# Kernel tuning notes

Measured on AMD Instinct MI355X. Metric: run time of the kernel, lower is better.

Reference implementation:

```python
import jax, jax.numpy as jnp
import numpy as np

N, E, G = 50000, 800000, 64
F_IN, H, R, C = 64, 64, 3, 10


def setup_inputs() -> dict:
    key = jax.random.key(0)
    ks = jax.random.split(key, 16)
    s = 0.1
    return dict(
        x=jax.random.normal(ks[0], (N, F_IN), jnp.float32),
        edge_index=jax.random.randint(ks[1], (2, E), 0, N, dtype=jnp.int32),
        edge_type=jax.random.randint(ks[2], (E,), 0, R, dtype=jnp.int32),
        graph_batch=jnp.sort(jax.random.randint(ks[3], (N,), 0, G, dtype=jnp.int32)),
        # FiLMConv params (per-relation lin: bias=False; per-relation film: bias=True)
        film_lin_W=jax.random.normal(ks[4], (R, F_IN, H), jnp.float32) * s,
        film_film_W=jax.random.normal(ks[5], (R, F_IN, 2 * H), jnp.float32) * s,
        film_film_b=jnp.zeros((R, 2 * H), jnp.float32),
        skip_W=jax.random.normal(ks[6], (F_IN, H), jnp.float32) * s,
        skip_film_W=jax.random.normal(ks[7], (F_IN, 2 * H), jnp.float32) * s,
        skip_film_b=jnp.zeros((2 * H,), jnp.float32),
        # GATConv params (heads=1, concat=True, lin bias=False, final bias=True)
        gat_W=jax.random.normal(ks[8], (F_IN, H), jnp.float32) * s,
        gat_att_src=jax.random.normal(ks[9], (H,), jnp.float32) * s,
        gat_att_dst=jax.random.normal(ks[10], (H,), jnp.float32) * s,
        gat_b=jnp.zeros((H,), jnp.float32),
        # classifier MLP
        lin_W=jax.random.normal(ks[11], (4 * H, H), jnp.float32) * s,
        lin_b=jnp.zeros((H,), jnp.float32),
        fc_W=jax.random.normal(ks[12], (H, C), jnp.float32) * s,
        fc_b=jnp.zeros((C,), jnp.float32),
    )


def _film_conv(x, edge_index, edge_type, lin_W, film_W, film_b,
               skip_W, skip_film_W, skip_film_b):
    # PyG FiLMConv, aggr='mean' per relation, act=relu.
    n, r, h = x.shape[0], lin_W.shape[0], skip_W.shape[1]
    src, dst = edge_index[0], edge_index[1]
    fs = x @ skip_film_W + skip_film_b                  # [N,2H]; split -> (beta, gamma)
    out = jax.nn.relu(fs[:, h:] * (x @ skip_W) + fs[:, :h])
    xr = jnp.einsum('nd,rdh->rnh', x, lin_W)            # [R,N,H]
    fm = jnp.einsum('nd,rdh->rnh', x, film_W) + film_b[:, None, :]  # [R,N,2H]
    beta, gamma = fm[..., :h], fm[..., h:]
    # each edge uses its own relation's lin/film params
    msg = jax.nn.relu(gamma[edge_type, dst] * xr[edge_type, src] + beta[edge_type, dst])  # [E,H]
    seg = dst * r + edge_type                            # per-(node,relation) mean
    cnt = jax.ops.segment_sum(jnp.ones_like(msg[:, 0]), seg, num_segments=n * r)
    denom = jnp.maximum(cnt[seg], 1.0)
    agg = jax.ops.segment_sum(msg / denom[:, None], dst, num_segments=n)
    return out + agg


def _gat_conv(x, edge_index, W, att_src, att_dst, b):
    # PyG GATConv, heads=1, negative_slope=0.2, add_self_loops=True.
    n = x.shape[0]
    xp = x @ W                                           # [N,H]
    loop = jnp.arange(n, dtype=edge_index.dtype)
    src = jnp.concatenate([edge_index[0], loop])
    dst = jnp.concatenate([edge_index[1], loop])
    e = jax.nn.leaky_relu((xp @ att_src)[src] + (xp @ att_dst)[dst], 0.2)  # [E+N]
    m = jax.ops.segment_max(e, dst, num_segments=n)
    alpha = jnp.exp(e - m[dst])
    denom = jax.ops.segment_sum(alpha, dst, num_segments=n)
    alpha = alpha / denom[dst]
    return jax.ops.segment_sum(alpha[:, None] * xp[src], dst, num_segments=n) + b


def reference(x, edge_index, edge_type, graph_batch,
              film_lin_W, film_film_W, film_film_b, skip_W, skip_film_W, skip_film_b,
              gat_W, gat_att_src, gat_att_dst, gat_b,
              lin_W, lin_b, fc_W, fc_b):
    out1 = jax.nn.relu(_film_conv(x, edge_index, edge_type, film_lin_W, film_film_W,
                                  film_film_b, skip_W, skip_film_W, skip_film_b))
    out2 = jax.nn.relu(_gat_conv(x, edge_index, gat_W, gat_att_src, gat_att_dst, gat_b))
    feats = jnp.concatenate([out1, out2], axis=-1)       # [N,2H]
    g = G
    cnt = jax.ops.segment_sum(jnp.ones_like(feats[:, 0]), graph_batch, num_segments=g)
    mx = jax.ops.segment_max(feats, graph_batch, num_segments=g)
    mx = jnp.where(cnt[:, None] > 0, mx, 0.0)
    mean = jax.ops.segment_sum(feats, graph_batch, num_segments=g) / jnp.maximum(cnt, 1.0)[:, None]
    pooled = jnp.concatenate([mx, mean], axis=-1)        # [G,4H]
    hidden = jax.nn.relu(pooled @ lin_W + lin_b)         # dropout = identity (eval)
    logits = hidden @ fc_W + fc_b
    return jax.nn.log_softmax(logits, axis=-1)
```

## Files before the change

### kernel.cpp

```cpp
#include <hip/hip_runtime.h>
#include <hip/hip_bf16.h>

#define NN 50000
#define EE 800000
#define GG 64
#define RR 3
#define CC 10
#define RPL 16
#define NBG 782
#define NBS 1563

typedef __attribute__((ext_vector_type(8))) short bf16x8;
typedef __attribute__((ext_vector_type(4))) float f32x4;

__device__ inline float leaky02(float x) { return x > 0.f ? x : 0.2f * x; }

__device__ inline void atomicMaxFPos(float* addr, float v) {
  atomicMax((int*)addr, __float_as_int(v));
}

__device__ inline unsigned short f2bf(float f) {
  __hip_bfloat16 b = __float2bfloat16(f);
  return *reinterpret_cast<unsigned short*>(&b);
}
__device__ inline float bf2f(unsigned short u) {
  return __uint_as_float(((unsigned int)u) << 16);
}

__global__ void wpack_k(const float* __restrict__ skip_film_W,
                        const float* __restrict__ skip_W,
                        const float* __restrict__ film_lin_W,
                        const float* __restrict__ film_film_W,
                        const float* __restrict__ gat_W,
                        const float* __restrict__ skip_film_b,
                        const float* __restrict__ film_film_b,
                        unsigned short* __restrict__ Wt,
                        float* __restrict__ bias) {
  int idx = blockIdx.x * 256 + threadIdx.x;
  if (idx >= 832 * 64 + 832) return;
  if (idx >= 832 * 64) {
    int c = idx - 832 * 64;
    float bv = 0.f;
    if (c < 128) bv = skip_film_b[c];
    else if (c >= 384 && c < 768) bv = film_film_b[c - 384];
    bias[c] = bv;
    return;
  }
  int c = idx >> 6, k = idx & 63;
  float v;
  if (c < 128)      v = skip_film_W[k * 128 + c];
  else if (c < 192) v = skip_W[k * 64 + (c - 128)];
  else if (c < 384) { int cc = c - 192, r = cc >> 6, h = cc & 63;
                      v = film_lin_W[(r * 64 + k) * 64 + h]; }
  else if (c < 768) { int cc = c - 384, r = cc >> 7, j = cc & 127;
                      v = film_film_W[(r * 64 + k) * 128 + j]; }
  else              v = gat_W[k * 64 + (c - 768)];
  Wt[idx] = f2bf(v);
}

__global__ __launch_bounds__(256) void fuse_k(const float* __restrict__ X,
    const unsigned short* __restrict__ Wt, const float* __restrict__ bias,
    const float* __restrict__ att_src, const float* __restrict__ att_dst,
    unsigned short* __restrict__ XP, unsigned short* __restrict__ XR,
    unsigned short* __restrict__ Ybg,
    unsigned short* __restrict__ S0b, float* __restrict__ as_,
    float* __restrict__ ad_,
    const int* __restrict__ ei, const int* __restrict__ et,
    int* __restrict__ fill4, int* __restrict__ sorted) {
  __shared__ __align__(16) unsigned short As[64][72];
  __shared__ __align__(16) unsigned short Bs[128][72];
  const int tid = threadIdx.x;

  if (blockIdx.x >= NBG) {
    int e = (blockIdx.x - NBG) * 512 + tid * 2;
    if (e < EE) {
      int2 s2 = *reinterpret_cast<const int2*>(ei + e);
      int2 d2 = *reinterpret_cast<const int2*>(ei + EE + e);
      int2 t2 = *reinterpret_cast<const int2*>(et + e);
      int slot = atomicAdd(&fill4[d2.x * 4 + t2.x], 1);
      if (slot < 32) sorted[d2.x * 96 + t2.x * 32 + slot] = s2.x;
      slot = atomicAdd(&fill4[d2.y * 4 + t2.y], 1);
      if (slot < 32) sorted[d2.y * 96 + t2.y * 32 + slot] = s2.y;
    }
    return;
  }

  const int row0 = blockIdx.x * 64;
  {
    int r = tid >> 2, c0 = (tid & 3) * 16;
    int gr = row0 + r;
    ushort4 o0 = {0,0,0,0}, o1 = {0,0,0,0}, o2 = {0,0,0,0}, o3 = {0,0,0,0};
    if (gr < NN) {
      const float4* p = reinterpret_cast<const float4*>(X + (size_t)gr * 64 + c0);
      float4 v0 = p[0], v1 = p[1], v2 = p[2], v3 = p[3];
      o0 = {f2bf(v0.x), f2bf(v0.y), f2bf(v0.z), f2bf(v0.w)};
      o1 = {f2bf(v1.x), f2bf(v1.y), f2bf(v1.z), f2bf(v1.w)};
      o2 = {f2bf(v2.x), f2bf(v2.y), f2bf(v2.z), f2bf(v2.w)};
      o3 = {f2bf(v3.x), f2bf(v3.y), f2bf(v3.z), f2bf(v3.w)};
    }
    *reinterpret_cast<ushort4*>(&As[r][c0])      = o0;
    *reinterpret_cast<ushort4*>(&As[r][c0 + 4])  = o1;
    *reinterpret_cast<ushort4*>(&As[r][c0 + 8])  = o2;
    *reinterpret_cast<ushort4*>(&As[r][c0 + 12]) = o3;
  }
  __syncthreads();

  const int w = tid >> 6, lane = tid & 63;
  const int m = lane & 15, q = lane >> 4;
  bf16x8 a0 = *reinterpret_cast<const bf16x8*>(&As[16 * w + m][q * 8]);
  bf16x8 a1 = *reinterpret_cast<const bf16x8*>(&As[16 * w + m][32 + q * 8]);
  const int rbase = row0 + 16 * w + q * 4;

  f32x4 t0[8], t1[4], t6[4];

  for (int tile = 0; tile < 7; tile++) {
    __syncthreads();
    int col0 = tile * 128;
    int width = (tile == 6) ? 64 : 128;
    {
      int c = tid >> 1, half = (tid & 1) * 32;
      if (c < width) {
        int gc = col0 + c;
        const uint4* p = reinterpret_cast<const uint4*>(Wt + (size_t)gc * 64 + half);
        uint4 v0 = p[0], v1 = p[1], v2 = p[2], v3 = p[3];
        *reinterpret_cast<uint4*>(&Bs[c][half])      = v0;
        *reinterpret_cast<uint4*>(&Bs[c][half + 8])  = v1;
        *reinterpret_cast<uint4*>(&Bs[c][half + 16]) = v2;
        *reinterpret_cast<uint4*>(&Bs[c][half + 24]) = v3;
      }
    }
    __syncthreads();
    #pragma unroll
    for (int ct = 0; ct < 8; ct++) {
      if (tile == 6 && ct >= 4) continue;
      bf16x8 b0 = *reinterpret_cast<const bf16x8*>(&Bs[ct * 16 + m][q * 8]);
      bf16x8 b1 = *reinterpret_cast<const bf16x8*>(&Bs[ct * 16 + m][32 + q * 8]);
      f32x4 acc = {0.f, 0.f, 0.f, 0.f};
      acc = __builtin_amdgcn_mfma_f32_16x16x32_bf16(a0, b0, acc, 0, 0, 0);
      acc = __builtin_amdgcn_mfma_f32_16x16x32_bf16(a1, b1, acc, 0, 0, 0);
      if (tile == 0) { t0[ct] = acc; continue; }
      if (tile == 1 && ct < 4) { t1[ct] = acc; continue; }
      if (tile == 6) t6[ct] = acc;
      int colm = ct * 16 + m;
      float bv = (tile >= 3 && tile <= 5) ? bias[col0 + colm] : 0.f;
      #pragma unroll
      for (int rg = 0; rg < 4; rg++) {
        int gr = rbase + rg;
        if (gr >= NN) continue;
        float v = acc[rg];
        if (tile == 1) {
          XR[(size_t)gr * 64 + (colm - 64)] = f2bf(v);
        } else if (tile == 2) {
          if (ct < 4) XR[((size_t)NN + gr) * 64 + colm]            = f2bf(v);
          else        XR[((size_t)2 * NN + gr) * 64 + (colm - 64)] = f2bf(v);
        } else if (tile <= 5) {
          Ybg[(size_t)gr * 384 + (col0 - 384) + colm] = f2bf(v + bv);
        } else {
          XP[(size_t)gr * 64 + colm] = f2bf(v);
        }
      }
    }
  }

  float pa[4] = {0.f, 0.f, 0.f, 0.f}, pd[4] = {0.f, 0.f, 0.f, 0.f};
  #pragma unroll
  for (int j = 0; j < 4; j++) {
    int h = 16 * j + m;
    float bb = bias[h];
    float bg = bias[64 + h];
    float asv = att_src[h];
    float adv = att_dst[h];
    #pragma unroll
    for (int rg = 0; rg < 4; rg++) {
      float so = fmaxf((t0[4 + j][rg] + bg) * t1[j][rg] + (t0[j][rg] + bb), 0.f);
      int gr = rbase + rg;
      if (gr < NN) S0b[(size_t)gr * 64 + h] = f2bf(so);
      pa[rg] += t6[j][rg] * asv;
      pd[rg] += t6[j][rg] * adv;
    }
  }
  #pragma unroll
  for (int ofs = 1; ofs < 16; ofs <<= 1) {
    #pragma unroll
    for (int rg = 0; rg < 4; rg++) {
      pa[rg] += __shfl_xor(pa[rg], ofs);
      pd[rg] += __shfl_xor(pd[rg], ofs);
    }
  }
  if (m == 0) {
    #pragma unroll
    for (int rg = 0; rg < 4; rg++) {
      int gr = rbase + rg;
      if (gr < NN) { as_[gr] = pa[rg]; ad_[gr] = pd[rg]; }
    }
  }
}

#define RPN 16

__global__ __launch_bounds__(256) void dst_k(const int* __restrict__ sorted,
    const int* __restrict__ fill4, const unsigned short* __restrict__ XP,
    const unsigned short* __restrict__ XR,
    const unsigned short* __restrict__ Ybg,
    const unsigned short* __restrict__ S0b,
    const float* __restrict__ as_, const float* __restrict__ ad_,
    const float* __restrict__ gat_b, const int* __restrict__ gb,
    float* __restrict__ pmax, float* __restrict__ psum,
    int* __restrict__ gstart, int* __restrict__ gend) {
  __shared__ int   s_pk[4][96];
  __shared__ float s_w [4][96];
  __shared__ int   s_d [4][4];
  __shared__ int   s_g[4];
  __shared__ float s_ad[4];
  __shared__ __align__(16) unsigned short s_rows[64][128];
  float* s_val = (float*)&s_rows[0][0];

  const int tid = threadIdx.x;
  const int wid = tid >> 6, h = tid & 63;
  const int n0 = blockIdx.x * 4;
  const int n  = n0 + wid;

  size_t rep = (size_t)(blockIdx.x & (RPL - 1)) * GG * 128;
  pmax += rep; psum += rep;

  if (tid < 16) {
    int wd = tid >> 2, t = tid & 3;
    if (t < 3) {
      int d = fill4[(n0 + wd) * 4 + t];
      s_d[wd][t] = d > 32 ? 32 : d;
    } else {
      s_g[wd]  = gb[n0 + wd];
      s_ad[wd] = ad_[n0 + wd];
    }
  }
  __syncthreads();

  for (int i = tid; i < 512; i += 256) {
    int wd = i >> 7, s = i & 127;
    if (s < 96) {
      int tt = s >> 5, j = s & 31;
      if (j < s_d[wd][tt]) {
        int cidx = (tt == 0) ? j
                 : (tt == 1) ? s_d[wd][0] + j
                             : s_d[wd][0] + s_d[wd][1] + j;
        int src = sorted[(size_t)(n0 + wd) * 96 + s];
        s_pk[wd][cidx] = src;
        s_w[wd][cidx]  = leaky02(as_[src] + s_ad[wd]);
      }
    }
  }
  __syncthreads();

  const int d0 = s_d[wid][0], d1 = s_d[wid][1], d2 = s_d[wid][2];
  const int sB = d0 + d1;
  const int deg = sB + d2;
  const float adn = s_ad[wid];
  float es = leaky02(as_[n] + adn);

  bool v1 = h < deg;
  bool v2 = h + 64 < deg;
  float e1 = v1 ? s_w[wid][h]      : -1e30f;
  float e2 = v2 ? s_w[wid][64 + h] : -1e30f;
  float mg = fmaxf(fmaxf(e1, e2), es);
  #pragma unroll
  for (int ofs = 1; ofs < 64; ofs <<= 1) mg = fmaxf(mg, __shfl_xor(mg, ofs));
  float w1 = v1 ? __expf(e1 - mg) : 0.f;
  float w2 = v2 ? __expf(e2 - mg) : 0.f;
  if (v1) s_w[wid][h] = w1;
  if (v2) s_w[wid][64 + h] = w2;
  float den = w1 + w2;
  #pragma unroll
  for (int ofs = 1; ofs < 64; ofs <<= 1) den += __shfl_xor(den, ofs);
  float ws = __expf(es - mg);
  den += ws;

  const float i0 = 1.f / (float)(d0 > 1 ? d0 : 1);
  const float i1 = 1.f / (float)(d1 > 1 ? d1 : 1);
  const float i2 = 1.f / (float)(d2 > 1 ? d2 : 1);
  const unsigned short* ybg = Ybg + (size_t)n * 384;
  const float b0p = bf2f(ybg[h])       * i0, g0p = bf2f(ybg[64 + h])  * i0;
  const float b1p = bf2f(ybg[128 + h]) * i1, g1p = bf2f(ybg[192 + h]) * i1;
  const float b2p = bf2f(ybg[256 + h]) * i2, g2p = bf2f(ybg[320 + h]) * i2;

  float S = ws * bf2f(XP[(size_t)n * 64 + h]);
  float f = 0.f;

  const int grp16 = tid >> 4, lane16 = tid & 15;
  int kA[4], kB[4], kD[4];
  #pragma unroll
  for (int k = 0; k < 4; k++) {
    kA[k] = s_d[k][0];
    kB[k] = kA[k] + s_d[k][1];
    kD[k] = kB[k] + s_d[k][2];
  }
  int dmax = max(max(kD[0], kD[1]), max(kD[2], kD[3]));
  int rounds = (dmax + RPN - 1) / RPN;

  for (int r = 0; r < rounds; r++) {
    int e0 = r * RPN;
    #pragma unroll
    for (int k = 0; k < 4; k++) {
      int jj = e0 + grp16;
      if (jj < kD[k]) {
        int src = s_pk[k][jj];
        int t = jj < kA[k] ? 0 : (jj < kB[k] ? 1 : 2);
        const unsigned short* row = (lane16 < 8)
            ? XP + (size_t)src * 64 + lane16 * 8
            : XR + ((size_t)t * NN + src) * 64 + (lane16 - 8) * 8;
        uint4 v = *reinterpret_cast<const uint4*>(row);
        *reinterpret_cast<uint4*>(&s_rows[16 * k + grp16][lane16 * 8]) = v;
      }
    }
    __syncthreads();
    const unsigned short* rowp = &s_rows[wid * RPN][0];
    int hi0 = min(e0 + RPN, d0);
    for (int i = e0; i < hi0; i++) {
      float wj = s_w[wid][i];
      int sr = i - e0;
      float xp = bf2f(rowp[sr * 128 + h]);
      float xr = bf2f(rowp[sr * 128 + 64 + h]);
      S += wj * xp;
      f += fmaxf(g0p * xr + b0p, 0.f);
    }
    int lo1 = max(e0, d0), hi1 = min(e0 + RPN, sB);
    for (int i = lo1; i < hi1; i++) {
      float wj = s_w[wid][i];
      int sr = i - e0;
      float xp = bf2f(rowp[sr * 128 + h]);
      float xr = bf2f(rowp[sr * 128 + 64 + h]);
      S += wj * xp;
      f += fmaxf(g1p * xr + b1p, 0.f);
    }
    int lo2 = max(e0, sB), hi2 = min(e0 + RPN, deg);
    for (int i = lo2; i < hi2; i++) {
      float wj = s_w[wid][i];
      int sr = i - e0;
      float xp = bf2f(rowp[sr * 128 + h]);
      float xr = bf2f(rowp[sr * 128 + 64 + h]);
      S += wj * xp;
      f += fmaxf(g2p * xr + b2p, 0.f);
    }
    __syncthreads();
  }

  float o1 = fmaxf(bf2f(S0b[(size_t)n * 64 + h]) + f, 0.f);
  float o2 = fmaxf(S / den + gat_b[h], 0.f);

  s_val[wid * 128 + h]      = o1;
  s_val[wid * 128 + 64 + h] = o2;
  if (h == 0) {
    int g = s_g[wid];
    if (n == 0 || gb[n - 1] != g)      gstart[g] = n;
    if (n == NN - 1 || gb[n + 1] != g) gend[g] = n;
  }
  __syncthreads();
  if (tid < 128) {
    int fch = tid;
    int curg = s_g[0];
    float v0 = s_val[fch];
    float mx = v0, sm = v0;
    #pragma unroll
    for (int j = 1; j < 4; j++) {
      float v = s_val[j * 128 + fch];
      if (s_g[j] == curg) { mx = fmaxf(mx, v); sm += v; }
      else {
        atomicMaxFPos(&pmax[curg * 128 + fch], mx);
        atomicAdd(&psum[curg * 128 + fch], sm);
        curg = s_g[j]; mx = v; sm = v;
      }
    }
    atomicMaxFPos(&pmax[curg * 128 + fch], mx);
    atomicAdd(&psum[curg * 128 + fch], sm);
  }
}

__global__ __launch_bounds__(64) void head_k(const float* __restrict__ pmax,
    const float* __restrict__ psum, const int* __restrict__ gstart,
    const int* __restrict__ gend,
    const float* __restrict__ lin_W, const float* __restrict__ lin_b,
    const float* __restrict__ fc_W, const float* __restrict__ fc_b,
    float* __restrict__ out) {
  __shared__ float p[256];
  __shared__ float hid[64];
  __shared__ float lg[CC];
  __shared__ float lse;
  int g = blockIdx.x, t = threadIdx.x;
  int s = gstart[g], e = gend[g];
  int cnt = (s <= e && s < NN && s >= 0) ? (e - s + 1) : 0;
  float invc = 1.f / (float)(cnt > 1 ? cnt : 1);
  for (int i = t; i < 256; i += 64) {
    if (i < 128) {
      float mx = 0.f;
      for (int r = 0; r < RPL; r++)
        mx = fmaxf(mx, pmax[((size_t)r * GG + g) * 128 + i]);
      p[i] = mx;
    } else {
      int f = i - 128;
      float sm = 0.f;
      for (int r = 0; r < RPL; r++)
        sm += psum[((size_t)r * GG + g) * 128 + f];
      p[i] = sm * invc;
    }
  }
  __syncthreads();
  float acc = lin_b[t];
  for (int k = 0; k < 256; k++) acc += p[k] * lin_W[k * 64 + t];
  hid[t] = fmaxf(acc, 0.f);
  __syncthreads();
  if (t < CC) {
    float a = fc_b[t];
    for (int k = 0; k < 64; k++) a += hid[k] * fc_W[k * CC + t];
    lg[t] = a;
  }
  __syncthreads();
  if (t == 0) {
    float mx = lg[0];
    for (int i = 1; i < CC; i++) mx = fmaxf(mx, lg[i]);
    float sum = 0.f;
    for (int i = 0; i < CC; i++) sum += expf(lg[i] - mx);
    lse = mx + logf(sum);
  }
  __syncthreads();
  if (t < CC) out[g * CC + t] = lg[t] - lse;
}

extern "C" void kernel_launch(void* const* d_in, const int* in_sizes, int n_in,
                              void* d_out, int out_size, void* d_ws, size_t ws_size,
                              hipStream_t stream) {
  const float* x            = (const float*)d_in[0];
  const int*   edge_index   = (const int*)d_in[1];
  const int*   edge_type    = (const int*)d_in[2];
  const int*   graph_batch  = (const int*)d_in[3];
  const float* film_lin_W   = (const float*)d_in[4];
  const float* film_film_W  = (const float*)d_in[5];
  const float* film_film_b  = (const float*)d_in[6];
  const float* skip_W       = (const float*)d_in[7];
  const float* skip_film_W  = (const float*)d_in[8];
  const float* skip_film_b  = (const float*)d_in[9];
  const float* gat_W        = (const float*)d_in[10];
  const float* att_src      = (const float*)d_in[11];
  const float* att_dst      = (const float*)d_in[12];
  const float* gat_b        = (const float*)d_in[13];
  const float* lin_W        = (const float*)d_in[14];
  const float* lin_b        = (const float*)d_in[15];
  const float* fc_W         = (const float*)d_in[16];
  const float* fc_b         = (const float*)d_in[17];
  float* out                = (float*)d_out;

  float* ws = (float*)d_ws;
  const size_t N = NN, G = GG;
  size_t oXP     = 0;
  size_t oXR     = N * 32;
  size_t oYbg    = oXR + N * 96;
  size_t oS0     = oYbg + N * 192;
  size_t oAs     = oS0 + N * 32;
  size_t oAd     = oAs + N;
  size_t oWt     = oAd + N;
  size_t oBias   = oWt + 832 * 32;
  size_t oPmax   = oBias + 832;
  size_t oPsum   = oPmax + (size_t)RPL * G * 128;
  size_t oGend   = oPsum + (size_t)RPL * G * 128;
  size_t oFill   = oGend + G;
  size_t oGstart = oFill + N * 4;
  size_t oSorted = oGstart + G;

  unsigned short* XP  = (unsigned short*)(ws + oXP);
  unsigned short* XR  = (unsigned short*)(ws + oXR);
  unsigned short* Ybg = (unsigned short*)(ws + oYbg);
  unsigned short* S0b = (unsigned short*)(ws + oS0);
  float* as_    = ws + oAs;
  float* ad_    = ws + oAd;
  unsigned short* Wt  = (unsigned short*)(ws + oWt);
  float* bias   = ws + oBias;
  float* pmax   = ws + oPmax;
  float* psum   = ws + oPsum;
  int*   gend   = (int*)(ws + oGend);
  int*   fill4  = (int*)(ws + oFill);
  int*   gstart = (int*)(ws + oGstart);
  int*   sorted = (int*)(ws + oSorted);

  size_t zeroFloats = oGstart - oPmax;
  hipMemsetAsync(pmax, 0, zeroFloats * sizeof(float), stream);

  wpack_k<<<212, 256, 0, stream>>>(skip_film_W, skip_W, film_lin_W,
                                   film_film_W, gat_W, skip_film_b,
                                   film_film_b, Wt, bias);
  fuse_k<<<NBG + NBS, 256, 0, stream>>>(x, Wt, bias, att_src, att_dst,
                                        XP, XR, Ybg, S0b, as_, ad_,
                                        edge_index, edge_type, fill4, sorted);
  dst_k<<<NN / 4, 256, 0, stream>>>(sorted, fill4, XP, XR, Ybg, S0b, as_, ad_,
                                    gat_b, graph_batch, pmax, psum,
                                    gstart, gend);
  head_k<<<GG, 64, 0, stream>>>(pmax, psum, gstart, gend,
                                lin_W, lin_b, fc_W, fc_b, out);
}
```

Before: 239.5 us.

## Fold memset into wpack, interleave GEMM/scatter blocks, 16-bit sorted indices, widen head

```diff
diff --git a/kernel.cpp b/kernel.cpp
--- a/kernel.cpp
+++ b/kernel.cpp
@@ -35,8 +35,13 @@
                         const float* __restrict__ skip_film_b,
                         const float* __restrict__ film_film_b,
                         unsigned short* __restrict__ Wt,
-                        float* __restrict__ bias) {
-  int idx = blockIdx.x * 256 + threadIdx.x;
+                        float* __restrict__ bias,
+                        float* __restrict__ zbase, int zN4) {
+  int tid0 = blockIdx.x * 256 + threadIdx.x;
+  float4 z4 = {0.f, 0.f, 0.f, 0.f};
+  for (int i = tid0; i < zN4; i += gridDim.x * 256)
+    reinterpret_cast<float4*>(zbase)[i] = z4;
+  int idx = tid0;
   if (idx >= 832 * 64 + 832) return;
   if (idx >= 832 * 64) {
     int c = idx - 832 * 64;
@@ -66,26 +71,30 @@
     unsigned short* __restrict__ S0b, float* __restrict__ as_,
     float* __restrict__ ad_,
     const int* __restrict__ ei, const int* __restrict__ et,
-    int* __restrict__ fill4, int* __restrict__ sorted) {
+    int* __restrict__ fill4, unsigned short* __restrict__ sorted) {
   __shared__ __align__(16) unsigned short As[64][72];
   __shared__ __align__(16) unsigned short Bs[128][72];
   const int tid = threadIdx.x;
-
-  if (blockIdx.x >= NBG) {
-    int e = (blockIdx.x - NBG) * 512 + tid * 2;
+  const int bid = blockIdx.x;
+
+  if (bid % 3 != 0) {
+    int sb = bid - bid / 3 - 1;
+    int e = sb * 512 + tid * 2;
     if (e < EE) {
       int2 s2 = *reinterpret_cast<const int2*>(ei + e);
       int2 d2 = *reinterpret_cast<const int2*>(ei + EE + e);
       int2 t2 = *reinterpret_cast<const int2*>(et + e);
       int slot = atomicAdd(&fill4[d2.x * 4 + t2.x], 1);
-      if (slot < 32) sorted[d2.x * 96 + t2.x * 32 + slot] = s2.x;
+      if (slot < 32)
+        sorted[(size_t)d2.x * 96 + t2.x * 32 + slot] = (unsigned short)s2.x;
       slot = atomicAdd(&fill4[d2.y * 4 + t2.y], 1);
-      if (slot < 32) sorted[d2.y * 96 + t2.y * 32 + slot] = s2.y;
+      if (slot < 32)
+        sorted[(size_t)d2.y * 96 + t2.y * 32 + slot] = (unsigned short)s2.y;
     }
     return;
   }
 
-  const int row0 = blockIdx.x * 64;
+  const int row0 = (bid / 3) * 64;
   {
     int r = tid >> 2, c0 = (tid & 3) * 16;
     int gr = row0 + r;
@@ -198,7 +207,7 @@
 
 #define RPN 16
 
-__global__ __launch_bounds__(256) void dst_k(const int* __restrict__ sorted,
+__global__ __launch_bounds__(256) void dst_k(const unsigned short* __restrict__ sorted,
     const int* __restrict__ fill4, const unsigned short* __restrict__ XP,
     const unsigned short* __restrict__ XR,
     const unsigned short* __restrict__ Ybg,
@@ -374,13 +383,14 @@
   }
 }
 
-__global__ __launch_bounds__(64) void head_k(const float* __restrict__ pmax,
+__global__ __launch_bounds__(256) void head_k(const float* __restrict__ pmax,
     const float* __restrict__ psum, const int* __restrict__ gstart,
     const int* __restrict__ gend,
     const float* __restrict__ lin_W, const float* __restrict__ lin_b,
     const float* __restrict__ fc_W, const float* __restrict__ fc_b,
     float* __restrict__ out) {
   __shared__ float p[256];
+  __shared__ float ph[4][64];
   __shared__ float hid[64];
   __shared__ float lg[CC];
   __shared__ float lse;
@@ -388,24 +398,33 @@
   int s = gstart[g], e = gend[g];
   int cnt = (s <= e && s < NN && s >= 0) ? (e - s + 1) : 0;
   float invc = 1.f / (float)(cnt > 1 ? cnt : 1);
-  for (int i = t; i < 256; i += 64) {
-    if (i < 128) {
-      float mx = 0.f;
-      for (int r = 0; r < RPL; r++)
-        mx = fmaxf(mx, pmax[((size_t)r * GG + g) * 128 + i]);
-      p[i] = mx;
-    } else {
-      int f = i - 128;
-      float sm = 0.f;
-      for (int r = 0; r < RPL; r++)
-        sm += psum[((size_t)r * GG + g) * 128 + f];
-      p[i] = sm * invc;
-    }
-  }
-  __syncthreads();
-  float acc = lin_b[t];
-  for (int k = 0; k < 256; k++) acc += p[k] * lin_W[k * 64 + t];
-  hid[t] = fmaxf(acc, 0.f);
+  if (t < 128) {
+    float mx = 0.f;
+    #pragma unroll
+    for (int r = 0; r < RPL; r++)
+      mx = fmaxf(mx, pmax[((size_t)r * GG + g) * 128 + t]);
+    p[t] = mx;
+  } else {
+    int f = t - 128;
+    float sm = 0.f;
+    #pragma unroll
+    for (int r = 0; r < RPL; r++)
+      sm += psum[((size_t)r * GG + g) * 128 + f];
+    p[t] = sm * invc;
+  }
+  __syncthreads();
+  {
+    int part = t >> 6, tt = t & 63;
+    float acc = 0.f;
+    int k0 = part * 64;
+    for (int k = k0; k < k0 + 64; k++) acc += p[k] * lin_W[k * 64 + tt];
+    ph[part][tt] = acc;
+  }
+  __syncthreads();
+  if (t < 64) {
+    float a = lin_b[t] + ph[0][t] + ph[1][t] + ph[2][t] + ph[3][t];
+    hid[t] = fmaxf(a, 0.f);
+  }
   __syncthreads();
   if (t < CC) {
     float a = fc_b[t];
@@ -477,20 +496,19 @@
   int*   gend   = (int*)(ws + oGend);
   int*   fill4  = (int*)(ws + oFill);
   int*   gstart = (int*)(ws + oGstart);
-  int*   sorted = (int*)(ws + oSorted);
-
-  size_t zeroFloats = oGstart - oPmax;
-  hipMemsetAsync(pmax, 0, zeroFloats * sizeof(float), stream);
+  unsigned short* sorted = (unsigned short*)(ws + oSorted);
+
+  int zN4 = (int)((oGstart - oPmax) / 4);
 
   wpack_k<<<212, 256, 0, stream>>>(skip_film_W, skip_W, film_lin_W,
                                    film_film_W, gat_W, skip_film_b,
-                                   film_film_b, Wt, bias);
+                                   film_film_b, Wt, bias, pmax, zN4);
   fuse_k<<<NBG + NBS, 256, 0, stream>>>(x, Wt, bias, att_src, att_dst,
                                         XP, XR, Ybg, S0b, as_, ad_,
                                         edge_index, edge_type, fill4, sorted);
   dst_k<<<NN / 4, 256, 0, stream>>>(sorted, fill4, XP, XR, Ybg, S0b, as_, ad_,
                                     gat_b, graph_batch, pmax, psum,
                                     gstart, gend);
-  head_k<<<GG, 64, 0, stream>>>(pmax, psum, gstart, gend,
-                                lin_W, lin_b, fc_W, fc_b, out);
-}
+  head_k<<<GG, 256, 0, stream>>>(pmax, psum, gstart, gend,
+                                 lin_W, lin_b, fc_W, fc_b, out);
+}
```

Result: no change. 235.9 us (-1.5%).
